# Kernel tuning notes

Measured on AMD Instinct MI355X. Metric: run time of the kernel, lower is better.

The kernel has to match this reference:

```python
import jax, jax.numpy as jnp
import numpy as np

H = 512      # hidden_size (hardcoded in __init__)
WD = 1024    # word_dim (hardcoded)
V = 4096     # len(i2w)+4
B, S, T = 256, 80, 28


def setup_inputs() -> dict:
    key = jax.random.key(0)
    ks = jax.random.split(key, 14)

    def gl(k, shape, fan_in):
        return (jax.random.normal(k, shape, jnp.float32) / np.sqrt(fan_in)).astype(jnp.float32)

    return {
        "encoder_last_hidden_state": jax.random.normal(ks[0], (1, B, H), jnp.float32),
        "encoder_output": jax.random.normal(ks[1], (B, S, H), jnp.float32),
        "targets": jax.random.randint(ks[2], (B, T), 0, V, dtype=jnp.int32),
        # embedding table
        "embedding": gl(ks[3], (V, WD), WD),
        # attention MLP (4 stacked linears, no activations, per the source)
        "W1": gl(ks[4], (2 * H, H), 2 * H), "b1": jnp.zeros((H,), jnp.float32),
        "W2": gl(ks[5], (H, H), H), "b2": jnp.zeros((H,), jnp.float32),
        "W3": gl(ks[6], (H, H), H), "b3": jnp.zeros((H,), jnp.float32),
        "W4": gl(ks[7], (H, H), H), "b4": jnp.zeros((H,), jnp.float32),
        "Ww": gl(ks[8], (H, 1), H),
        # GRU (input = hidden_size + word_dim = 1536), PyTorch gate order r,z,n
        "W_ih": gl(ks[9], (3 * H, H + WD), H + WD), "b_ih": jnp.zeros((3 * H,), jnp.float32),
        "W_hh": gl(ks[10], (3 * H, H), H), "b_hh": jnp.zeros((3 * H,), jnp.float32),
        # output projection
        "Wo": gl(ks[11], (H, V), H), "bo": jnp.zeros((V,), jnp.float32),
    }


def reference(encoder_last_hidden_state, encoder_output, targets, embedding,
              W1, b1, W2, b2, W3, b3, W4, b4, Ww,
              W_ih, b_ih, W_hh, b_hh, Wo, bo):
    n_steps = targets.shape[1] - 1  # seq_len - 1 decode steps

    def attention(h, enc):
        # h: (B,H) decoder hidden; enc: (B,S,H)
        hs = jnp.broadcast_to(h[:, None, :], enc.shape)
        m = jnp.concatenate([enc, hs], axis=-1)          # (B,S,2H)
        x = m @ W1 + b1
        x = x @ W2 + b2
        x = x @ W3 + b3
        x = x @ W4 + b4
        attw = jax.nn.softmax((x @ Ww)[..., 0], axis=1)  # (B,S)
        return jnp.einsum('bs,bsh->bh', attw, enc)       # context (B,H)

    def gru_cell(x, h):
        gi = x @ W_ih.T + b_ih
        gh = h @ W_hh.T + b_hh
        ir, iz, inn = jnp.split(gi, 3, axis=-1)
        hr, hz, hn = jnp.split(gh, 3, axis=-1)
        r = jax.nn.sigmoid(ir + hr)
        z = jax.nn.sigmoid(iz + hz)
        n = jnp.tanh(inn + r * hn)
        return (1.0 - z) * n + z * h

    h0 = encoder_last_hidden_state[0]                    # (B,H)
    w0 = jnp.ones((encoder_output.shape[0],), jnp.int32) # <BOS> = 1

    def step(carry, _):
        h, w = carry
        emb = embedding[w]                               # (B,WD)
        ctx = attention(h, encoder_output)               # (B,H)
        x = jnp.concatenate([emb, ctx], axis=-1)         # (B,WD+H)
        hn = gru_cell(x, h)
        logits = hn @ Wo + bo                            # (B,V)
        wn = jnp.argmax(logits, axis=-1).astype(jnp.int32)
        return (hn, wn), logits

    _, logits_seq = jax.lax.scan(step, (h0, w0), None, length=n_steps)
    seq_logProb = jnp.swapaxes(logits_seq, 0, 1)         # (B, T-1, V)
    seq_predictions = jnp.argmax(seq_logProb, axis=-1)
    return seq_logProb, seq_predictions
```

## Files before the change

kernel.cpp:

```cpp
#include <hip/hip_runtime.h>

#define B_ 256
#define S_ 80
#define H_ 512
#define V_ 4096
#define NSTEP 27

typedef unsigned short u16;
typedef __attribute__((ext_vector_type(8))) short short8v;
typedef __attribute__((ext_vector_type(4))) float f32x4;
typedef __attribute__((ext_vector_type(4))) unsigned short ushort4v;

#define MFMA_(a,b,c) __builtin_amdgcn_mfma_f32_16x16x32_bf16(a,b,c,0,0,0)
#define MFMA3(acc, ah, al, bh, bl) do{ acc = MFMA_(ah,bh,acc); acc = MFMA_(ah,bl,acc); acc = MFMA_(al,bh,acc);}while(0)

__device__ __forceinline__ unsigned fkey(float v){
    unsigned u = __float_as_uint(v);
    return (u & 0x80000000u) ? ~u : (u | 0x80000000u);
}
__device__ __forceinline__ u16 bf16_rne(float f){
    unsigned u = __float_as_uint(f);
    return (u16)((u + 0x7FFFu + ((u >> 16) & 1u)) >> 16);
}
__device__ __forceinline__ void split_f4(float4 v, ushort4v& hi, ushort4v& lo){
    float arr[4] = {v.x, v.y, v.z, v.w};
    ushort4v h, l;
#pragma unroll
    for (int i = 0; i < 4; ++i){
        u16 hb = bf16_rne(arr[i]);
        h[i] = hb;
        l[i] = bf16_rne(arr[i] - __uint_as_float(((unsigned)hb) << 16));
    }
    hi = h; lo = l;
}

__global__ __launch_bounds__(64) void matvec512(const float* __restrict__ W,
                                                const float* __restrict__ v,
                                                float* __restrict__ out){
    int row = blockIdx.x, lane = threadIdx.x;
    const float* wr = W + row * 512;
    float s = 0.f;
#pragma unroll
    for (int i = 0; i < 8; ++i) s += wr[lane + 64*i] * v[lane + 64*i];
#pragma unroll
    for (int off = 32; off; off >>= 1) s += __shfl_xor(s, off);
    if (lane == 0) out[row] = s;
}

__global__ __launch_bounds__(512) void attn_ctx(const float* __restrict__ enc,
                                                const float* __restrict__ weff,
                                                float* __restrict__ ctx){
    __shared__ float att[S_];
    int b = blockIdx.x, tid = threadIdx.x;
    int wv = tid >> 6, lane = tid & 63;
    float w8[8];
#pragma unroll
    for (int i = 0; i < 8; ++i) w8[i] = weff[lane + 64*i];
    const float* eb = enc + (size_t)b * (S_*H_);
    for (int s = wv; s < S_; s += 8){
        const float* e = eb + s*512;
        float acc = 0.f;
#pragma unroll
        for (int i = 0; i < 8; ++i) acc += e[lane + 64*i] * w8[i];
#pragma unroll
        for (int off = 32; off; off >>= 1) acc += __shfl_xor(acc, off);
        if (lane == 0) att[s] = acc;
    }
    __syncthreads();
    if (tid == 0){
        float mx = att[0];
        for (int s = 1; s < S_; ++s) mx = fmaxf(mx, att[s]);
        float sum = 0.f;
        for (int s = 0; s < S_; ++s){ float e = expf(att[s] - mx); att[s] = e; sum += e; }
        float inv = 1.f / sum;
        for (int s = 0; s < S_; ++s) att[s] *= inv;
    }
    __syncthreads();
    float a = 0.f;
    for (int s = 0; s < S_; ++s) a += att[s] * eb[s*512 + tid];
    ctx[b*512 + tid] = a;
}

template<int TM>
__global__ __launch_bounds__(256) void gemm_abt(const float* __restrict__ A, int lda,
                                                const float* __restrict__ Bm, int ldb,
                                                const float* __restrict__ bias,
                                                float* __restrict__ C, int ldc, int K){
    constexpr int RPT = TM / 16;
    __shared__ float As[16][TM + 4];
    __shared__ float Bs[16][64 + 4];
    int m0 = blockIdx.x * TM, n0 = blockIdx.y * 64;
    int tid = threadIdx.x;
    int lk = tid & 15, lr = tid >> 4;
    int tx = tid & 15, ty = tid >> 4;
    float c[RPT][4] = {};
    for (int k0 = 0; k0 < K; k0 += 16){
#pragma unroll
        for (int i = 0; i < RPT; ++i)
            As[lk][lr*RPT + i] = A[(size_t)(m0 + lr*RPT + i)*lda + k0 + lk];
#pragma unroll
        for (int i = 0; i < 4; ++i)
            Bs[lk][lr*4 + i] = Bm[(size_t)(n0 + lr*4 + i)*ldb + k0 + lk];
        __syncthreads();
#pragma unroll
        for (int k = 0; k < 16; ++k){
            float b4[4];
            *(float4*)b4 = *(const float4*)&Bs[k][tx*4];
#pragma unroll
            for (int i = 0; i < RPT; ++i){
                float a = As[k][ty*RPT + i];
#pragma unroll
                for (int j = 0; j < 4; ++j) c[i][j] += a * b4[j];
            }
        }
        __syncthreads();
    }
#pragma unroll
    for (int j = 0; j < 4; ++j){
        float bb = bias ? bias[n0 + tx*4 + j] : 0.f;
#pragma unroll
        for (int i = 0; i < RPT; ++i)
            C[(size_t)(m0 + ty*RPT + i)*ldc + n0 + tx*4 + j] = c[i][j] + bb;
    }
}

__global__ __launch_bounds__(256) void prep_all(
    const float* __restrict__ Whh, const float* __restrict__ Wo,
    const float* __restrict__ emb, const float* __restrict__ Wih,
    const float* __restrict__ elhs,
    u16* __restrict__ WhhHi, u16* __restrict__ WhhLo,
    u16* __restrict__ WoThi, u16* __restrict__ WoTlo,
    u16* __restrict__ EmbHi, u16* __restrict__ EmbLo,
    u16* __restrict__ WihLHi, u16* __restrict__ WihLLo,
    u16* __restrict__ Sh, u16* __restrict__ Sl,
    unsigned* __restrict__ zp, int nz)
{
    __shared__ float T[64][65];
    int b = blockIdx.x, tid = threadIdx.x;
    if (b < 768){
        int idx = (b*256 + tid)*4;
        float4 v = *(const float4*)&Whh[idx];
        ushort4v h,l; split_f4(v,h,l);
        *(ushort4v*)&WhhHi[idx]=h; *(ushort4v*)&WhhLo[idx]=l;
    } else if (b < 1280){
        int lb = b - 768;
        int k0 = (lb & 7)*64, n0 = (lb >> 3)*64;
#pragma unroll
        for (int i = 0; i < 16; ++i){
            int idx = tid + i*256;
            int kk = idx >> 6, nn = idx & 63;
            T[kk][nn] = Wo[(size_t)(k0+kk)*4096 + n0+nn];
        }
        __syncthreads();
#pragma unroll
        for (int i = 0; i < 16; ++i){
            int idx = tid + i*256;
            int nn = idx >> 6, kk = idx & 63;
            float v = T[kk][nn];
            u16 hi = bf16_rne(v);
            u16 lo = bf16_rne(v - __uint_as_float(((unsigned)hi) << 16));
            size_t o = (size_t)(n0+nn)*512 + k0+kk;
            WoThi[o] = hi; WoTlo[o] = lo;
        }
    } else if (b < 5376){
        int idx = ((b-1280)*256 + tid)*4;
        float4 v = *(const float4*)&emb[idx];
        ushort4v h,l; split_f4(v,h,l);
        *(ushort4v*)&EmbHi[idx]=h; *(ushort4v*)&EmbLo[idx]=l;
    } else if (b < 6912){
        int id = ((b-5376)*256 + tid)*4;
        int r = id >> 10, c = id & 1023;
        float4 v = *(const float4*)&Wih[(size_t)r*1536 + c];
        ushort4v h,l; split_f4(v,h,l);
        *(ushort4v*)&WihLHi[id]=h; *(ushort4v*)&WihLLo[id]=l;
    } else if (b < 7040){
        int idx = ((b-6912)*256 + tid)*4;
        float4 v = *(const float4*)&elhs[idx];
        ushort4v h,l; split_f4(v,h,l);
        *(ushort4v*)&Sh[idx]=h; *(ushort4v*)&Sl[idx]=l;
    } else {
        int i = ((b-7040)*256 + tid)*4;
        if (i < nz){ zp[i]=0u; zp[i+1]=0u; zp[i+2]=0u; zp[i+3]=0u; }
    }
}

__global__ __launch_bounds__(256) void eproj_u16(const u16* __restrict__ Ahi, const u16* __restrict__ Alo,
                                                 const u16* __restrict__ Bhi, const u16* __restrict__ Blo,
                                                 float* __restrict__ C){
    __shared__ u16 Ah[2048], Al[2048], Bh[4096], Bl[4096];
    int n0 = blockIdx.x * 128, m0 = blockIdx.y * 64;
    int tid = threadIdx.x, lane = tid & 63, wid = tid >> 6;
    int wy = wid & 1, wx = wid >> 1;
    int l15 = lane & 15, rg = lane >> 4, lk = rg * 8;
    int ar = tid >> 2, ak8 = (tid & 3) * 8;

    const u16* gAh = Ahi + (size_t)(m0 + ar)*1024 + ak8;
    const u16* gAl = Alo + (size_t)(m0 + ar)*1024 + ak8;
    const u16* gBh0 = Bhi + (size_t)(n0 + ar)*1024 + ak8;
    const u16* gBl0 = Blo + (size_t)(n0 + ar)*1024 + ak8;
    const u16* gBh1 = gBh0 + (size_t)64*1024;
    const u16* gBl1 = gBl0 + (size_t)64*1024;

    short8v rAh = *(const short8v*)gAh;
    short8v rAl = *(const short8v*)gAl;
    short8v rBh0 = *(const short8v*)gBh0;
    short8v rBl0 = *(const short8v*)gBl0;
    short8v rBh1 = *(const short8v*)gBh1;
    short8v rBl1 = *(const short8v*)gBl1;

    f32x4 acc[2][4] = {};
    for (int k0 = 0; k0 < 1024; k0 += 32){
        __syncthreads();
        *(short8v*)&Ah[tid*8] = rAh;
        *(short8v*)&Al[tid*8] = rAl;
        *(short8v*)&Bh[tid*8] = rBh0;
        *(short8v*)&Bl[tid*8] = rBl0;
        *(short8v*)&Bh[2048 + tid*8] = rBh1;
        *(short8v*)&Bl[2048 + tid*8] = rBl1;
        __syncthreads();
        if (k0 + 32 < 1024){
            rAh  = *(const short8v*)(gAh + k0 + 32);
            rAl  = *(const short8v*)(gAl + k0 + 32);
            rBh0 = *(const short8v*)(gBh0 + k0 + 32);
            rBl0 = *(const short8v*)(gBl0 + k0 + 32);
            rBh1 = *(const short8v*)(gBh1 + k0 + 32);
            rBl1 = *(const short8v*)(gBl1 + k0 + 32);
        }
        short8v afh[2], afl[2];
        afh[0] = *(const short8v*)&Ah[(wy*32 +  0 + l15)*32 + lk];
        afh[1] = *(const short8v*)&Ah[(wy*32 + 16 + l15)*32 + lk];
        afl[0] = *(const short8v*)&Al[(wy*32 +  0 + l15)*32 + lk];
        afl[1] = *(const short8v*)&Al[(wy*32 + 16 + l15)*32 + lk];
#pragma unroll
        for (int nf = 0; nf < 4; ++nf){
            short8v bfh = *(const short8v*)&Bh[(wx*64 + nf*16 + l15)*32 + lk];
            short8v bfl = *(const short8v*)&Bl[(wx*64 + nf*16 + l15)*32 + lk];
            MFMA3(acc[0][nf], afh[0], afl[0], bfh, bfl);
            MFMA3(acc[1][nf], afh[1], afl[1], bfh, bfl);
        }
    }
    int col0 = n0 + wx*64 + l15;
#pragma unroll
    for (int mf = 0; mf < 2; ++mf)
#pragma unroll
        for (int r = 0; r < 4; ++r){
            int row = m0 + wy*32 + mf*16 + rg*4 + r;
#pragma unroll
            for (int nf = 0; nf < 4; ++nf)
                C[(size_t)row*1536 + col0 + nf*16] = acc[mf][nf][r];
        }
}


__global__ __launch_bounds__(128) void gru_pointwise(
    const float* __restrict__ gh, const float* __restrict__ Eproj,
    const float* __restrict__ gictx, const float* __restrict__ bhh,
    const float* __restrict__ hprev, float* __restrict__ hnext,
    u16* __restrict__ Sh, u16* __restrict__ Sl,
    const unsigned long long* __restrict__ Pprev,
    float* __restrict__ preds, int t)
{
    int tid = threadIdx.x;
    int row = blockIdx.x;
    int jj = tid * 4;
    int w = 1;
    if (t > 0){
        w = 4095 - (int)(Pprev[row] & 0xFFFFFFFFull);
        if (w < 0) w = 0; if (w > 4095) w = 4095;
        if (tid == 0) preds[row*NSTEP + (t-1)] = (float)w;
    }
    const float* gr = gh + (size_t)row * 1536;
    const float* ep = Eproj + (size_t)w * 1536;
    const float* gc = gictx + (size_t)row * 1536;
    float4 g0 = *(const float4*)&gr[jj];
    float4 g1 = *(const float4*)&gr[512 + jj];
    float4 g2 = *(const float4*)&gr[1024 + jj];
    float4 e0 = *(const float4*)&ep[jj];
    float4 e1 = *(const float4*)&ep[512 + jj];
    float4 e2 = *(const float4*)&ep[1024 + jj];
    float4 c0 = *(const float4*)&gc[jj];
    float4 c1 = *(const float4*)&gc[512 + jj];
    float4 c2 = *(const float4*)&gc[1024 + jj];
    float4 b0 = *(const float4*)&bhh[jj];
    float4 b1 = *(const float4*)&bhh[512 + jj];
    float4 b2 = *(const float4*)&bhh[1024 + jj];
    float4 ho = *(const float4*)&hprev[(size_t)row*512 + jj];
    const float* G0 = (const float*)&g0; const float* G1 = (const float*)&g1;
    const float* G2 = (const float*)&g2;
    const float* E0 = (const float*)&e0; const float* E1 = (const float*)&e1;
    const float* E2 = (const float*)&e2;
    const float* C0 = (const float*)&c0; const float* C1 = (const float*)&c1;
    const float* C2 = (const float*)&c2;
    const float* B0 = (const float*)&b0; const float* B1 = (const float*)&b1;
    const float* B2 = (const float*)&b2;
    const float* HO = (const float*)&ho;
    float4 res;
    float* R = (float*)&res;
#pragma unroll
    for (int i = 0; i < 4; ++i){
        float gir = E0[i] + C0[i] + G0[i] + B0[i];
        float giz = E1[i] + C1[i] + G1[i] + B1[i];
        float gin = E2[i] + C2[i];
        float rr = 1.f / (1.f + expf(-gir));
        float zz = 1.f / (1.f + expf(-giz));
        float nn = tanhf(gin + rr * (G2[i] + B2[i]));
        R[i] = (1.f - zz)*nn + zz*HO[i];
    }
    size_t o = (size_t)row*512 + jj;
    *(float4*)&hnext[o] = res;
    ushort4v h4, l4; split_f4(res, h4, l4);
    *(ushort4v*)&Sh[o] = h4;
    *(ushort4v*)&Sl[o] = l4;
}

__global__ __launch_bounds__(256) void step_mm(
    const u16* __restrict__ Ahg, const u16* __restrict__ Alg,
    const u16* __restrict__ WoHi, const u16* __restrict__ WoLo,
    const u16* __restrict__ WhhHi, const u16* __restrict__ WhhLo,
    const float* __restrict__ bo,
    float* __restrict__ logits, unsigned long long* __restrict__ Pcur,
    float* __restrict__ gh_out, int n_logits)
{
    __shared__ u16 Ah[2][2048], Al[2][2048], Bh[2][2048], Bl[2][2048];
    int m0 = blockIdx.x * 64;
    int nt = blockIdx.y;
    bool isL = nt < n_logits;
    int nbase = (isL ? nt : nt - n_logits) * 64;
    const u16* Bhg = isL ? WoHi : WhhHi;
    const u16* Blg = isL ? WoLo : WhhLo;
    int tid = threadIdx.x, lane = tid & 63, wid = tid >> 6;
    int wy = wid & 1, wx = wid >> 1;
    int l15 = lane & 15, rg = lane >> 4, lk = rg * 8;
    int sr = tid >> 2, sk8 = (tid & 3) * 8;

    const u16* gAh = Ahg + (size_t)(m0 + sr)*512 + sk8;
    const u16* gAl = Alg + (size_t)(m0 + sr)*512 + sk8;
    const u16* gBh = Bhg + (size_t)(nbase + sr)*512 + sk8;
    const u16* gBl = Blg + (size_t)(nbase + sr)*512 + sk8;

    *(short8v*)&Ah[0][tid*8] = *(const short8v*)gAh;
    *(short8v*)&Al[0][tid*8] = *(const short8v*)gAl;
    *(short8v*)&Bh[0][tid*8] = *(const short8v*)gBh;
    *(short8v*)&Bl[0][tid*8] = *(const short8v*)gBl;
    short8v r1a = *(const short8v*)(gAh + 32), r1b = *(const short8v*)(gAl + 32);
    short8v r1c = *(const short8v*)(gBh + 32), r1d = *(const short8v*)(gBl + 32);
    short8v r2a = *(const short8v*)(gAh + 64), r2b = *(const short8v*)(gAl + 64);
    short8v r2c = *(const short8v*)(gBh + 64), r2d = *(const short8v*)(gBl + 64);
    __syncthreads();

    f32x4 acc[2][2] = {};
    int p = 0;
    for (int k0 = 0; k0 < 512; k0 += 32){
        if (k0 + 32 < 512){
            *(short8v*)&Ah[p^1][tid*8] = r1a;
            *(short8v*)&Al[p^1][tid*8] = r1b;
            *(short8v*)&Bh[p^1][tid*8] = r1c;
            *(short8v*)&Bl[p^1][tid*8] = r1d;
            r1a = r2a; r1b = r2b; r1c = r2c; r1d = r2d;
            if (k0 + 96 < 512){
                r2a = *(const short8v*)(gAh + k0 + 96);
                r2b = *(const short8v*)(gAl + k0 + 96);
                r2c = *(const short8v*)(gBh + k0 + 96);
                r2d = *(const short8v*)(gBl + k0 + 96);
            }
        }
        short8v afh0 = *(const short8v*)&Ah[p][(wy*32 +  0 + l15)*32 + lk];
        short8v afh1 = *(const short8v*)&Ah[p][(wy*32 + 16 + l15)*32 + lk];
        short8v afl0 = *(const short8v*)&Al[p][(wy*32 +  0 + l15)*32 + lk];
        short8v afl1 = *(const short8v*)&Al[p][(wy*32 + 16 + l15)*32 + lk];
        short8v bfh0 = *(const short8v*)&Bh[p][(wx*32 +  0 + l15)*32 + lk];
        short8v bfh1 = *(const short8v*)&Bh[p][(wx*32 + 16 + l15)*32 + lk];
        short8v bfl0 = *(const short8v*)&Bl[p][(wx*32 +  0 + l15)*32 + lk];
        short8v bfl1 = *(const short8v*)&Bl[p][(wx*32 + 16 + l15)*32 + lk];
        MFMA3(acc[0][0], afh0, afl0, bfh0, bfl0);
        MFMA3(acc[0][1], afh0, afl0, bfh1, bfl1);
        MFMA3(acc[1][0], afh1, afl1, bfh0, bfl0);
        MFMA3(acc[1][1], afh1, afl1, bfh1, bfl1);
        __syncthreads();
        p ^= 1;
    }

    int col0 = nbase + wx*32 + l15;
    if (isL){
        float bo0 = bo[col0], bo1 = bo[col0 + 16];
#pragma unroll
        for (int mf = 0; mf < 2; ++mf){
#pragma unroll
            for (int r = 0; r < 4; ++r){
                int row = m0 + wy*32 + mf*16 + rg*4 + r;
                float v0 = acc[mf][0][r] + bo0;
                float v1 = acc[mf][1][r] + bo1;
                float* crow = logits + (size_t)row * (NSTEP * (size_t)V_);
                crow[col0]      = v0;
                crow[col0 + 16] = v1;
                unsigned long long k0_ = ((unsigned long long)fkey(v0) << 32) | (unsigned)(4095 - col0);
                unsigned long long k1_ = ((unsigned long long)fkey(v1) << 32) | (unsigned)(4095 - (col0+16));
                unsigned long long best = k0_ > k1_ ? k0_ : k1_;
#pragma unroll
                for (int off = 1; off < 16; off <<= 1){
                    unsigned long long o = __shfl_xor(best, off);
                    if (o > best) best = o;
                }
                if (l15 == 0) atomicMax(&Pcur[row], best);
            }
        }
    } else {
#pragma unroll
        for (int mf = 0; mf < 2; ++mf)
#pragma unroll
            for (int r = 0; r < 4; ++r){
                int row = m0 + wy*32 + mf*16 + rg*4 + r;
                gh_out[(size_t)row*1536 + col0]      = acc[mf][0][r];
                gh_out[(size_t)row*1536 + col0 + 16] = acc[mf][1][r];
            }
    }
}

__global__ __launch_bounds__(256) void final_pred(const unsigned long long* __restrict__ P,
                                                  float* __restrict__ preds){
    int b = threadIdx.x;
    int w = 4095 - (int)(P[b] & 0xFFFFFFFFull);
    if (w < 0) w = 0; if (w > 4095) w = 4095;
    preds[b*NSTEP + (NSTEP-1)] = (float)w;
}

extern "C" void kernel_launch(void* const* d_in, const int* in_sizes, int n_in,
                              void* d_out, int out_size, void* d_ws, size_t ws_size,
                              hipStream_t stream){
    const float* elhs = (const float*)d_in[0];
    const float* enc  = (const float*)d_in[1];
    const float* emb  = (const float*)d_in[3];
    const float* W1   = (const float*)d_in[4];
    const float* W2   = (const float*)d_in[6];
    const float* W3   = (const float*)d_in[8];
    const float* W4   = (const float*)d_in[10];
    const float* Ww   = (const float*)d_in[12];
    const float* Wih  = (const float*)d_in[13];
    const float* bih  = (const float*)d_in[14];
    const float* Whh  = (const float*)d_in[15];
    const float* bhh  = (const float*)d_in[16];
    const float* Wo   = (const float*)d_in[17];
    const float* bo   = (const float*)d_in[18];

    float* out = (float*)d_out;
    float* preds = out + (size_t)B_ * NSTEP * V_;

    float* ws = (float*)d_ws;
    float* Eproj  = ws;  ws += (size_t)V_ * 1536;
    float* gictx  = ws;  ws += (size_t)B_ * 1536;
    float* ctx    = ws;  ws += B_ * H_;
    float* t1     = ws;  ws += 512;
    float* t2     = ws;  ws += 512;
    float* weff   = ws;  ws += 512;
    float* Hf     = ws;  ws += 2 * B_ * H_;
    float* ghbuf  = ws;  ws += B_ * 1536;
    u16* WoT_hi = (u16*)ws;  ws += (size_t)V_ * 512 / 2;
    u16* WoT_lo = (u16*)ws;  ws += (size_t)V_ * 512 / 2;
    u16* WhhHi  = (u16*)ws;  ws += 1536 * 512 / 2;
    u16* WhhLo  = (u16*)ws;  ws += 1536 * 512 / 2;
    u16* Sh     = (u16*)ws;  ws += B_ * H_ / 2;
    u16* Sl     = (u16*)ws;  ws += B_ * H_ / 2;
    unsigned long long* P = (unsigned long long*)ws;

    u16* EmbHi  = (u16*)d_out;
    u16* EmbLo  = EmbHi + (size_t)V_*1024;
    u16* WihLHi = EmbLo + (size_t)V_*1024;
    u16* WihLLo = WihLHi + (size_t)1536*1024;

    prep_all<<<7054, 256, 0, stream>>>(Whh, Wo, emb, Wih, elhs,
                                       WhhHi, WhhLo, WoT_hi, WoT_lo,
                                       EmbHi, EmbLo, WihLHi, WihLLo,
                                       Sh, Sl, (unsigned*)P, NSTEP*256*2);

    matvec512<<<512, 64, 0, stream>>>(W4, Ww, t1);
    matvec512<<<512, 64, 0, stream>>>(W3, t1, t2);
    matvec512<<<512, 64, 0, stream>>>(W2, t2, t1);
    matvec512<<<512, 64, 0, stream>>>(W1, t1, weff);
    attn_ctx<<<B_, 512, 0, stream>>>(enc, weff, ctx);
    { dim3 g(B_/32, 1536/64);
      gemm_abt<32><<<g, 256, 0, stream>>>(ctx, 512, Wih + 1024, 1536, bih, gictx, 1536, 512); }
    { dim3 g(1536/128, V_/64);
      eproj_u16<<<g, 256, 0, stream>>>(EmbHi, EmbLo, WihLHi, WihLLo, Eproj); }

    { dim3 g(4, 24);
      step_mm<<<g, 256, 0, stream>>>(Sh, Sl, WoT_hi, WoT_lo, WhhHi, WhhLo, bo,
                                     out, P, ghbuf, 0); }

    for (int t = 0; t < NSTEP; ++t){
        const float* hr = (t == 0) ? elhs : (Hf + (size_t)((t-1) & 1) * (B_*H_));
        float*       hw = Hf + (size_t)(t & 1) * (B_*H_);
        const unsigned long long* Pprev = P + (size_t)(t > 0 ? t-1 : 0) * 256;
        gru_pointwise<<<256, 128, 0, stream>>>(ghbuf, Eproj, gictx, bhh, hr, hw,
                                               Sh, Sl, Pprev, preds, t);
        dim3 g(4, 64 + 24);
        step_mm<<<g, 256, 0, stream>>>(Sh, Sl, WoT_hi, WoT_lo, WhhHi, WhhLo, bo,
                                       out + (size_t)t * V_, P + (size_t)t*256, ghbuf, 64);
    }
    final_pred<<<1, 256, 0, stream>>>(P + (size_t)(NSTEP-1)*256, preds);
}
```

Measured before the change: 746.5 us.

## Merge front-end kernels: fold attention matvec chain into prep and fuse setup GEMMs

The four matvec launches that collapse the attention MLP into a single weight vector now run in one extra block of the prep kernel. The ctx-projection GEMM, the embedding projection GEMM (retiled to 128x128) and the first hidden-to-hidden step_mm are combined into one heterogeneous launch. The goal is to cut launch count and serialization in the setup phase. The trade-off is that the weff chain runs in a single block, which can end up on the critical path, and branch-divergent blocks inside one kernel may load-balance unevenly.

After: 841.5 us. +12.7%, slower.

```diff
diff --git a/kernel.cpp b/kernel.cpp
--- a/kernel.cpp
+++ b/kernel.cpp
@@ -34,105 +34,19 @@
     hi = h; lo = l;
 }
 
-__global__ __launch_bounds__(64) void matvec512(const float* __restrict__ W,
-                                                const float* __restrict__ v,
-                                                float* __restrict__ out){
-    int row = blockIdx.x, lane = threadIdx.x;
-    const float* wr = W + row * 512;
-    float s = 0.f;
-#pragma unroll
-    for (int i = 0; i < 8; ++i) s += wr[lane + 64*i] * v[lane + 64*i];
-#pragma unroll
-    for (int off = 32; off; off >>= 1) s += __shfl_xor(s, off);
-    if (lane == 0) out[row] = s;
-}
-
-__global__ __launch_bounds__(512) void attn_ctx(const float* __restrict__ enc,
-                                                const float* __restrict__ weff,
-                                                float* __restrict__ ctx){
-    __shared__ float att[S_];
-    int b = blockIdx.x, tid = threadIdx.x;
-    int wv = tid >> 6, lane = tid & 63;
-    float w8[8];
-#pragma unroll
-    for (int i = 0; i < 8; ++i) w8[i] = weff[lane + 64*i];
-    const float* eb = enc + (size_t)b * (S_*H_);
-    for (int s = wv; s < S_; s += 8){
-        const float* e = eb + s*512;
-        float acc = 0.f;
-#pragma unroll
-        for (int i = 0; i < 8; ++i) acc += e[lane + 64*i] * w8[i];
-#pragma unroll
-        for (int off = 32; off; off >>= 1) acc += __shfl_xor(acc, off);
-        if (lane == 0) att[s] = acc;
-    }
-    __syncthreads();
-    if (tid == 0){
-        float mx = att[0];
-        for (int s = 1; s < S_; ++s) mx = fmaxf(mx, att[s]);
-        float sum = 0.f;
-        for (int s = 0; s < S_; ++s){ float e = expf(att[s] - mx); att[s] = e; sum += e; }
-        float inv = 1.f / sum;
-        for (int s = 0; s < S_; ++s) att[s] *= inv;
-    }
-    __syncthreads();
-    float a = 0.f;
-    for (int s = 0; s < S_; ++s) a += att[s] * eb[s*512 + tid];
-    ctx[b*512 + tid] = a;
-}
-
-template<int TM>
-__global__ __launch_bounds__(256) void gemm_abt(const float* __restrict__ A, int lda,
-                                                const float* __restrict__ Bm, int ldb,
-                                                const float* __restrict__ bias,
-                                                float* __restrict__ C, int ldc, int K){
-    constexpr int RPT = TM / 16;
-    __shared__ float As[16][TM + 4];
-    __shared__ float Bs[16][64 + 4];
-    int m0 = blockIdx.x * TM, n0 = blockIdx.y * 64;
-    int tid = threadIdx.x;
-    int lk = tid & 15, lr = tid >> 4;
-    int tx = tid & 15, ty = tid >> 4;
-    float c[RPT][4] = {};
-    for (int k0 = 0; k0 < K; k0 += 16){
-#pragma unroll
-        for (int i = 0; i < RPT; ++i)
-            As[lk][lr*RPT + i] = A[(size_t)(m0 + lr*RPT + i)*lda + k0 + lk];
-#pragma unroll
-        for (int i = 0; i < 4; ++i)
-            Bs[lk][lr*4 + i] = Bm[(size_t)(n0 + lr*4 + i)*ldb + k0 + lk];
-        __syncthreads();
-#pragma unroll
-        for (int k = 0; k < 16; ++k){
-            float b4[4];
-            *(float4*)b4 = *(const float4*)&Bs[k][tx*4];
-#pragma unroll
-            for (int i = 0; i < RPT; ++i){
-                float a = As[k][ty*RPT + i];
-#pragma unroll
-                for (int j = 0; j < 4; ++j) c[i][j] += a * b4[j];
-            }
-        }
-        __syncthreads();
-    }
-#pragma unroll
-    for (int j = 0; j < 4; ++j){
-        float bb = bias ? bias[n0 + tx*4 + j] : 0.f;
-#pragma unroll
-        for (int i = 0; i < RPT; ++i)
-            C[(size_t)(m0 + ty*RPT + i)*ldc + n0 + tx*4 + j] = c[i][j] + bb;
-    }
-}
-
-__global__ __launch_bounds__(256) void prep_all(
+__global__ __launch_bounds__(256) void prep_front(
     const float* __restrict__ Whh, const float* __restrict__ Wo,
     const float* __restrict__ emb, const float* __restrict__ Wih,
     const float* __restrict__ elhs,
+    const float* __restrict__ W1, const float* __restrict__ W2,
+    const float* __restrict__ W3, const float* __restrict__ W4,
+    const float* __restrict__ Ww,
     u16* __restrict__ WhhHi, u16* __restrict__ WhhLo,
     u16* __restrict__ WoThi, u16* __restrict__ WoTlo,
     u16* __restrict__ EmbHi, u16* __restrict__ EmbLo,
     u16* __restrict__ WihLHi, u16* __restrict__ WihLLo,
     u16* __restrict__ Sh, u16* __restrict__ Sl,
+    float* __restrict__ weff,
     unsigned* __restrict__ zp, int nz)
 {
     __shared__ float T[64][65];
@@ -178,79 +92,300 @@
         float4 v = *(const float4*)&elhs[idx];
         ushort4v h,l; split_f4(v,h,l);
         *(ushort4v*)&Sh[idx]=h; *(ushort4v*)&Sl[idx]=l;
-    } else {
+    } else if (b < 7054){
         int i = ((b-7040)*256 + tid)*4;
         if (i < nz){ zp[i]=0u; zp[i+1]=0u; zp[i+2]=0u; zp[i+3]=0u; }
-    }
-}
-
-__global__ __launch_bounds__(256) void eproj_u16(const u16* __restrict__ Ahi, const u16* __restrict__ Alo,
-                                                 const u16* __restrict__ Bhi, const u16* __restrict__ Blo,
-                                                 float* __restrict__ C){
-    __shared__ u16 Ah[2048], Al[2048], Bh[4096], Bl[4096];
-    int n0 = blockIdx.x * 128, m0 = blockIdx.y * 64;
+    } else {
+        float* vb0 = &T[0][0];
+        float* vb1 = vb0 + 512;
+        for (int i = tid; i < 512; i += 256) vb0[i] = Ww[i];
+        __syncthreads();
+        const float* Ws[4] = {W4, W3, W2, W1};
+        for (int s = 0; s < 4; ++s){
+            const float* src = (s & 1) ? vb1 : vb0;
+            float* dst = (s & 1) ? vb0 : vb1;
+            for (int r = tid; r < 512; r += 256){
+                const float* wr = Ws[s] + (size_t)r*512;
+                float acc = 0.f;
+                for (int k = 0; k < 512; k += 4){
+                    float4 wv = *(const float4*)&wr[k];
+                    acc += wv.x*src[k] + wv.y*src[k+1] + wv.z*src[k+2] + wv.w*src[k+3];
+                }
+                dst[r] = acc;
+            }
+            __syncthreads();
+        }
+        for (int i = tid; i < 512; i += 256) weff[i] = vb0[i];
+    }
+}
+
+__global__ __launch_bounds__(512) void attn_ctx(const float* __restrict__ enc,
+                                                const float* __restrict__ weff,
+                                                float* __restrict__ ctx){
+    __shared__ float att[S_];
+    int b = blockIdx.x, tid = threadIdx.x;
+    int wv = tid >> 6, lane = tid & 63;
+    float w8[8];
+#pragma unroll
+    for (int i = 0; i < 8; ++i) w8[i] = weff[lane + 64*i];
+    const float* eb = enc + (size_t)b * (S_*H_);
+    for (int s = wv; s < S_; s += 8){
+        const float* e = eb + s*512;
+        float acc = 0.f;
+#pragma unroll
+        for (int i = 0; i < 8; ++i) acc += e[lane + 64*i] * w8[i];
+#pragma unroll
+        for (int off = 32; off; off >>= 1) acc += __shfl_xor(acc, off);
+        if (lane == 0) att[s] = acc;
+    }
+    __syncthreads();
+    if (tid == 0){
+        float mx = att[0];
+        for (int s = 1; s < S_; ++s) mx = fmaxf(mx, att[s]);
+        float sum = 0.f;
+        for (int s = 0; s < S_; ++s){ float e = expf(att[s] - mx); att[s] = e; sum += e; }
+        float inv = 1.f / sum;
+        for (int s = 0; s < S_; ++s) att[s] *= inv;
+    }
+    __syncthreads();
+    float a = 0.f;
+    for (int s = 0; s < S_; ++s) a += att[s] * eb[s*512 + tid];
+    ctx[b*512 + tid] = a;
+}
+
+__device__ __forceinline__ void step_mm_body(char* smem, int m0, int nt, int n_logits,
+    const u16* __restrict__ Ahg, const u16* __restrict__ Alg,
+    const u16* __restrict__ WoHi, const u16* __restrict__ WoLo,
+    const u16* __restrict__ WhhHi, const u16* __restrict__ WhhLo,
+    const float* __restrict__ bo,
+    float* __restrict__ logits, unsigned long long* __restrict__ Pcur,
+    float* __restrict__ gh_out)
+{
+    u16 (*Ah)[2048] = (u16(*)[2048])(smem);
+    u16 (*Al)[2048] = (u16(*)[2048])(smem + 8192);
+    u16 (*Bh)[2048] = (u16(*)[2048])(smem + 16384);
+    u16 (*Bl)[2048] = (u16(*)[2048])(smem + 24576);
+    bool isL = nt < n_logits;
+    int nbase = (isL ? nt : nt - n_logits) * 64;
+    const u16* Bhg = isL ? WoHi : WhhHi;
+    const u16* Blg = isL ? WoLo : WhhLo;
     int tid = threadIdx.x, lane = tid & 63, wid = tid >> 6;
     int wy = wid & 1, wx = wid >> 1;
     int l15 = lane & 15, rg = lane >> 4, lk = rg * 8;
-    int ar = tid >> 2, ak8 = (tid & 3) * 8;
-
-    const u16* gAh = Ahi + (size_t)(m0 + ar)*1024 + ak8;
-    const u16* gAl = Alo + (size_t)(m0 + ar)*1024 + ak8;
-    const u16* gBh0 = Bhi + (size_t)(n0 + ar)*1024 + ak8;
-    const u16* gBl0 = Blo + (size_t)(n0 + ar)*1024 + ak8;
-    const u16* gBh1 = gBh0 + (size_t)64*1024;
-    const u16* gBl1 = gBl0 + (size_t)64*1024;
-
-    short8v rAh = *(const short8v*)gAh;
-    short8v rAl = *(const short8v*)gAl;
-    short8v rBh0 = *(const short8v*)gBh0;
-    short8v rBl0 = *(const short8v*)gBl0;
-    short8v rBh1 = *(const short8v*)gBh1;
-    short8v rBl1 = *(const short8v*)gBl1;
-
-    f32x4 acc[2][4] = {};
-    for (int k0 = 0; k0 < 1024; k0 += 32){
+    int sr = tid >> 2, sk8 = (tid & 3) * 8;
+
+    const u16* gAh = Ahg + (size_t)(m0 + sr)*512 + sk8;
+    const u16* gAl = Alg + (size_t)(m0 + sr)*512 + sk8;
+    const u16* gBh = Bhg + (size_t)(nbase + sr)*512 + sk8;
+    const u16* gBl = Blg + (size_t)(nbase + sr)*512 + sk8;
+
+    *(short8v*)&Ah[0][tid*8] = *(const short8v*)gAh;
+    *(short8v*)&Al[0][tid*8] = *(const short8v*)gAl;
+    *(short8v*)&Bh[0][tid*8] = *(const short8v*)gBh;
+    *(short8v*)&Bl[0][tid*8] = *(const short8v*)gBl;
+    short8v r1a = *(const short8v*)(gAh + 32), r1b = *(const short8v*)(gAl + 32);
+    short8v r1c = *(const short8v*)(gBh + 32), r1d = *(const short8v*)(gBl + 32);
+    short8v r2a = *(const short8v*)(gAh + 64), r2b = *(const short8v*)(gAl + 64);
+    short8v r2c = *(const short8v*)(gBh + 64), r2d = *(const short8v*)(gBl + 64);
+    __syncthreads();
+
+    f32x4 acc[2][2] = {};
+    int p = 0;
+    for (int k0 = 0; k0 < 512; k0 += 32){
+        if (k0 + 32 < 512){
+            *(short8v*)&Ah[p^1][tid*8] = r1a;
+            *(short8v*)&Al[p^1][tid*8] = r1b;
+            *(short8v*)&Bh[p^1][tid*8] = r1c;
+            *(short8v*)&Bl[p^1][tid*8] = r1d;
+            r1a = r2a; r1b = r2b; r1c = r2c; r1d = r2d;
+            if (k0 + 96 < 512){
+                r2a = *(const short8v*)(gAh + k0 + 96);
+                r2b = *(const short8v*)(gAl + k0 + 96);
+                r2c = *(const short8v*)(gBh + k0 + 96);
+                r2d = *(const short8v*)(gBl + k0 + 96);
+            }
+        }
+        short8v afh0 = *(const short8v*)&Ah[p][(wy*32 +  0 + l15)*32 + lk];
+        short8v afh1 = *(const short8v*)&Ah[p][(wy*32 + 16 + l15)*32 + lk];
+        short8v afl0 = *(const short8v*)&Al[p][(wy*32 +  0 + l15)*32 + lk];
+        short8v afl1 = *(const short8v*)&Al[p][(wy*32 + 16 + l15)*32 + lk];
+        short8v bfh0 = *(const short8v*)&Bh[p][(wx*32 +  0 + l15)*32 + lk];
+        short8v bfh1 = *(const short8v*)&Bh[p][(wx*32 + 16 + l15)*32 + lk];
+        short8v bfl0 = *(const short8v*)&Bl[p][(wx*32 +  0 + l15)*32 + lk];
+        short8v bfl1 = *(const short8v*)&Bl[p][(wx*32 + 16 + l15)*32 + lk];
+        MFMA3(acc[0][0], afh0, afl0, bfh0, bfl0);
+        MFMA3(acc[0][1], afh0, afl0, bfh1, bfl1);
+        MFMA3(acc[1][0], afh1, afl1, bfh0, bfl0);
+        MFMA3(acc[1][1], afh1, afl1, bfh1, bfl1);
         __syncthreads();
-        *(short8v*)&Ah[tid*8] = rAh;
-        *(short8v*)&Al[tid*8] = rAl;
-        *(short8v*)&Bh[tid*8] = rBh0;
-        *(short8v*)&Bl[tid*8] = rBl0;
-        *(short8v*)&Bh[2048 + tid*8] = rBh1;
-        *(short8v*)&Bl[2048 + tid*8] = rBl1;
-        __syncthreads();
-        if (k0 + 32 < 1024){
-            rAh  = *(const short8v*)(gAh + k0 + 32);
-            rAl  = *(const short8v*)(gAl + k0 + 32);
-            rBh0 = *(const short8v*)(gBh0 + k0 + 32);
-            rBl0 = *(const short8v*)(gBl0 + k0 + 32);
-            rBh1 = *(const short8v*)(gBh1 + k0 + 32);
-            rBl1 = *(const short8v*)(gBl1 + k0 + 32);
-        }
-        short8v afh[2], afl[2];
-        afh[0] = *(const short8v*)&Ah[(wy*32 +  0 + l15)*32 + lk];
-        afh[1] = *(const short8v*)&Ah[(wy*32 + 16 + l15)*32 + lk];
-        afl[0] = *(const short8v*)&Al[(wy*32 +  0 + l15)*32 + lk];
-        afl[1] = *(const short8v*)&Al[(wy*32 + 16 + l15)*32 + lk];
-#pragma unroll
-        for (int nf = 0; nf < 4; ++nf){
-            short8v bfh = *(const short8v*)&Bh[(wx*64 + nf*16 + l15)*32 + lk];
-            short8v bfl = *(const short8v*)&Bl[(wx*64 + nf*16 + l15)*32 + lk];
-            MFMA3(acc[0][nf], afh[0], afl[0], bfh, bfl);
-            MFMA3(acc[1][nf], afh[1], afl[1], bfh, bfl);
-        }
-    }
-    int col0 = n0 + wx*64 + l15;
-#pragma unroll
-    for (int mf = 0; mf < 2; ++mf)
-#pragma unroll
-        for (int r = 0; r < 4; ++r){
-            int row = m0 + wy*32 + mf*16 + rg*4 + r;
-#pragma unroll
-            for (int nf = 0; nf < 4; ++nf)
-                C[(size_t)row*1536 + col0 + nf*16] = acc[mf][nf][r];
-        }
-}
-
+        p ^= 1;
+    }
+
+    int col0 = nbase + wx*32 + l15;
+    if (isL){
+        float bo0 = bo[col0], bo1 = bo[col0 + 16];
+#pragma unroll
+        for (int mf = 0; mf < 2; ++mf){
+#pragma unroll
+            for (int r = 0; r < 4; ++r){
+                int row = m0 + wy*32 + mf*16 + rg*4 + r;
+                float v0 = acc[mf][0][r] + bo0;
+                float v1 = acc[mf][1][r] + bo1;
+                float* crow = logits + (size_t)row * (NSTEP * (size_t)V_);
+                crow[col0]      = v0;
+                crow[col0 + 16] = v1;
+                unsigned long long k0_ = ((unsigned long long)fkey(v0) << 32) | (unsigned)(4095 - col0);
+                unsigned long long k1_ = ((unsigned long long)fkey(v1) << 32) | (unsigned)(4095 - (col0+16));
+                unsigned long long best = k0_ > k1_ ? k0_ : k1_;
+#pragma unroll
+                for (int off = 1; off < 16; off <<= 1){
+                    unsigned long long o = __shfl_xor(best, off);
+                    if (o > best) best = o;
+                }
+                if (l15 == 0) atomicMax(&Pcur[row], best);
+            }
+        }
+    } else {
+#pragma unroll
+        for (int mf = 0; mf < 2; ++mf)
+#pragma unroll
+            for (int r = 0; r < 4; ++r){
+                int row = m0 + wy*32 + mf*16 + rg*4 + r;
+                gh_out[(size_t)row*1536 + col0]      = acc[mf][0][r];
+                gh_out[(size_t)row*1536 + col0 + 16] = acc[mf][1][r];
+            }
+    }
+}
+
+__global__ __launch_bounds__(256) void front3(
+    const u16* __restrict__ EmbHi, const u16* __restrict__ EmbLo,
+    const u16* __restrict__ WihLHi, const u16* __restrict__ WihLLo,
+    float* __restrict__ Eproj,
+    const float* __restrict__ ctx, const float* __restrict__ WihR,
+    const float* __restrict__ bih, float* __restrict__ gictx,
+    const u16* __restrict__ Sh0, const u16* __restrict__ Sl0,
+    const u16* __restrict__ WhhHi, const u16* __restrict__ WhhLo,
+    float* __restrict__ gh0)
+{
+    __shared__ __align__(16) char smem[32768];
+    int b = blockIdx.x, tid = threadIdx.x;
+    if (b < 384){
+        int bn = b % 12, bm = b / 12;
+        int n0 = bn * 128, m0 = bm * 128;
+        int lane = tid & 63, wid = tid >> 6;
+        int wy = wid & 1, wx = wid >> 1;
+        int l15 = lane & 15, rg = lane >> 4, lk = rg * 8;
+        u16* Ah = (u16*)smem;
+        u16* Al = (u16*)(smem + 8192);
+        u16* Bh = (u16*)(smem + 16384);
+        u16* Bl = (u16*)(smem + 24576);
+        const u16* gA[2][2]; const u16* gB[2][2];
+#pragma unroll
+        for (int j = 0; j < 2; ++j){
+            int s = tid + j*256;
+            int row = s >> 2, k8 = (s & 3)*8;
+            gA[0][j] = EmbHi + (size_t)(m0+row)*1024 + k8;
+            gA[1][j] = EmbLo + (size_t)(m0+row)*1024 + k8;
+            gB[0][j] = WihLHi + (size_t)(n0+row)*1024 + k8;
+            gB[1][j] = WihLLo + (size_t)(n0+row)*1024 + k8;
+        }
+        short8v rA[2][2], rB[2][2];
+#pragma unroll
+        for (int h = 0; h < 2; ++h)
+#pragma unroll
+            for (int j = 0; j < 2; ++j){
+                rA[h][j] = *(const short8v*)gA[h][j];
+                rB[h][j] = *(const short8v*)gB[h][j];
+            }
+        f32x4 acc[4][4] = {};
+        for (int k0 = 0; k0 < 1024; k0 += 32){
+            __syncthreads();
+#pragma unroll
+            for (int j = 0; j < 2; ++j){
+                int s8 = (tid + j*256)*8;
+                *(short8v*)&Ah[s8] = rA[0][j];
+                *(short8v*)&Al[s8] = rA[1][j];
+                *(short8v*)&Bh[s8] = rB[0][j];
+                *(short8v*)&Bl[s8] = rB[1][j];
+            }
+            __syncthreads();
+            if (k0 + 32 < 1024){
+#pragma unroll
+                for (int h = 0; h < 2; ++h)
+#pragma unroll
+                    for (int j = 0; j < 2; ++j){
+                        rA[h][j] = *(const short8v*)(gA[h][j] + k0 + 32);
+                        rB[h][j] = *(const short8v*)(gB[h][j] + k0 + 32);
+                    }
+            }
+            short8v afh[4], afl[4];
+#pragma unroll
+            for (int mf = 0; mf < 4; ++mf){
+                afh[mf] = *(const short8v*)&Ah[(wy*64 + mf*16 + l15)*32 + lk];
+                afl[mf] = *(const short8v*)&Al[(wy*64 + mf*16 + l15)*32 + lk];
+            }
+#pragma unroll
+            for (int nf = 0; nf < 4; ++nf){
+                short8v bfh = *(const short8v*)&Bh[(wx*64 + nf*16 + l15)*32 + lk];
+                short8v bfl = *(const short8v*)&Bl[(wx*64 + nf*16 + l15)*32 + lk];
+#pragma unroll
+                for (int mf = 0; mf < 4; ++mf)
+                    MFMA3(acc[mf][nf], afh[mf], afl[mf], bfh, bfl);
+            }
+        }
+        int col0 = n0 + wx*64 + l15;
+#pragma unroll
+        for (int mf = 0; mf < 4; ++mf)
+#pragma unroll
+            for (int r = 0; r < 4; ++r){
+                int row = m0 + wy*64 + mf*16 + rg*4 + r;
+#pragma unroll
+                for (int nf = 0; nf < 4; ++nf)
+                    Eproj[(size_t)row*1536 + col0 + nf*16] = acc[mf][nf][r];
+            }
+    } else if (b < 576){
+        int lb = b - 384;
+        int m0 = (lb & 7) * 32, n0 = (lb >> 3) * 64;
+        float (*As)[36] = (float(*)[36])smem;
+        float (*Bs)[68] = (float(*)[68])(smem + 2304);
+        int lk = tid & 15, lr = tid >> 4;
+        int tx = tid & 15, ty = tid >> 4;
+        float c[2][4] = {};
+        for (int k0 = 0; k0 < 512; k0 += 16){
+#pragma unroll
+            for (int i = 0; i < 2; ++i)
+                As[lk][lr*2 + i] = ctx[(size_t)(m0 + lr*2 + i)*512 + k0 + lk];
+#pragma unroll
+            for (int i = 0; i < 4; ++i)
+                Bs[lk][lr*4 + i] = WihR[(size_t)(n0 + lr*4 + i)*1536 + k0 + lk];
+            __syncthreads();
+#pragma unroll
+            for (int k = 0; k < 16; ++k){
+                float b4[4];
+                *(float4*)b4 = *(const float4*)&Bs[k][tx*4];
+#pragma unroll
+                for (int i = 0; i < 2; ++i){
+                    float a = As[k][ty*2 + i];
+#pragma unroll
+                    for (int j = 0; j < 4; ++j) c[i][j] += a * b4[j];
+                }
+            }
+            __syncthreads();
+        }
+#pragma unroll
+        for (int j = 0; j < 4; ++j){
+            float bb = bih[n0 + tx*4 + j];
+#pragma unroll
+            for (int i = 0; i < 2; ++i)
+                gictx[(size_t)(m0 + ty*2 + i)*1536 + n0 + tx*4 + j] = c[i][j] + bb;
+        }
+    } else {
+        int lb = b - 576;
+        step_mm_body(smem, (lb & 3)*64, lb >> 2, 0,
+                     Sh0, Sl0, nullptr, nullptr, WhhHi, WhhLo,
+                     nullptr, nullptr, nullptr, gh0);
+    }
+}
 
 __global__ __launch_bounds__(128) void gru_pointwise(
     const float* __restrict__ gh, const float* __restrict__ Eproj,
@@ -321,99 +456,9 @@
     float* __restrict__ logits, unsigned long long* __restrict__ Pcur,
     float* __restrict__ gh_out, int n_logits)
 {
-    __shared__ u16 Ah[2][2048], Al[2][2048], Bh[2][2048], Bl[2][2048];
-    int m0 = blockIdx.x * 64;
-    int nt = blockIdx.y;
-    bool isL = nt < n_logits;
-    int nbase = (isL ? nt : nt - n_logits) * 64;
-    const u16* Bhg = isL ? WoHi : WhhHi;
-    const u16* Blg = isL ? WoLo : WhhLo;
-    int tid = threadIdx.x, lane = tid & 63, wid = tid >> 6;
-    int wy = wid & 1, wx = wid >> 1;
-    int l15 = lane & 15, rg = lane >> 4, lk = rg * 8;
-    int sr = tid >> 2, sk8 = (tid & 3) * 8;
-
-    const u16* gAh = Ahg + (size_t)(m0 + sr)*512 + sk8;
-    const u16* gAl = Alg + (size_t)(m0 + sr)*512 + sk8;
-    const u16* gBh = Bhg + (size_t)(nbase + sr)*512 + sk8;
-    const u16* gBl = Blg + (size_t)(nbase + sr)*512 + sk8;
-
-    *(short8v*)&Ah[0][tid*8] = *(const short8v*)gAh;
-    *(short8v*)&Al[0][tid*8] = *(const short8v*)gAl;
-    *(short8v*)&Bh[0][tid*8] = *(const short8v*)gBh;
-    *(short8v*)&Bl[0][tid*8] = *(const short8v*)gBl;
-    short8v r1a = *(const short8v*)(gAh + 32), r1b = *(const short8v*)(gAl + 32);
-    short8v r1c = *(const short8v*)(gBh + 32), r1d = *(const short8v*)(gBl + 32);
-    short8v r2a = *(const short8v*)(gAh + 64), r2b = *(const short8v*)(gAl + 64);
-    short8v r2c = *(const short8v*)(gBh + 64), r2d = *(const short8v*)(gBl + 64);
-    __syncthreads();
-
-    f32x4 acc[2][2] = {};
-    int p = 0;
-    for (int k0 = 0; k0 < 512; k0 += 32){
-        if (k0 + 32 < 512){
-            *(short8v*)&Ah[p^1][tid*8] = r1a;
-            *(short8v*)&Al[p^1][tid*8] = r1b;
-            *(short8v*)&Bh[p^1][tid*8] = r1c;
-            *(short8v*)&Bl[p^1][tid*8] = r1d;
-            r1a = r2a; r1b = r2b; r1c = r2c; r1d = r2d;
-            if (k0 + 96 < 512){
-                r2a = *(const short8v*)(gAh + k0 + 96);
-                r2b = *(const short8v*)(gAl + k0 + 96);
-                r2c = *(const short8v*)(gBh + k0 + 96);
-                r2d = *(const short8v*)(gBl + k0 + 96);
-            }
-        }
-        short8v afh0 = *(const short8v*)&Ah[p][(wy*32 +  0 + l15)*32 + lk];
-        short8v afh1 = *(const short8v*)&Ah[p][(wy*32 + 16 + l15)*32 + lk];
-        short8v afl0 = *(const short8v*)&Al[p][(wy*32 +  0 + l15)*32 + lk];
-        short8v afl1 = *(const short8v*)&Al[p][(wy*32 + 16 + l15)*32 + lk];
-        short8v bfh0 = *(const short8v*)&Bh[p][(wx*32 +  0 + l15)*32 + lk];
-        short8v bfh1 = *(const short8v*)&Bh[p][(wx*32 + 16 + l15)*32 + lk];
-        short8v bfl0 = *(const short8v*)&Bl[p][(wx*32 +  0 + l15)*32 + lk];
-        short8v bfl1 = *(const short8v*)&Bl[p][(wx*32 + 16 + l15)*32 + lk];
-        MFMA3(acc[0][0], afh0, afl0, bfh0, bfl0);
-        MFMA3(acc[0][1], afh0, afl0, bfh1, bfl1);
-        MFMA3(acc[1][0], afh1, afl1, bfh0, bfl0);
-        MFMA3(acc[1][1], afh1, afl1, bfh1, bfl1);
-        __syncthreads();
-        p ^= 1;
-    }
-
-    int col0 = nbase + wx*32 + l15;
-    if (isL){
-        float bo0 = bo[col0], bo1 = bo[col0 + 16];
-#pragma unroll
-        for (int mf = 0; mf < 2; ++mf){
-#pragma unroll
-            for (int r = 0; r < 4; ++r){
-                int row = m0 + wy*32 + mf*16 + rg*4 + r;
-                float v0 = acc[mf][0][r] + bo0;
-                float v1 = acc[mf][1][r] + bo1;
-                float* crow = logits + (size_t)row * (NSTEP * (size_t)V_);
-                crow[col0]      = v0;
-                crow[col0 + 16] = v1;
-                unsigned long long k0_ = ((unsigned long long)fkey(v0) << 32) | (unsigned)(4095 - col0);
-                unsigned long long k1_ = ((unsigned long long)fkey(v1) << 32) | (unsigned)(4095 - (col0+16));
-                unsigned long long best = k0_ > k1_ ? k0_ : k1_;
-#pragma unroll
-                for (int off = 1; off < 16; off <<= 1){
-                    unsigned long long o = __shfl_xor(best, off);
-                    if (o > best) best = o;
-                }
-                if (l15 == 0) atomicMax(&Pcur[row], best);
-            }
-        }
-    } else {
-#pragma unroll
-        for (int mf = 0; mf < 2; ++mf)
-#pragma unroll
-            for (int r = 0; r < 4; ++r){
-                int row = m0 + wy*32 + mf*16 + rg*4 + r;
-                gh_out[(size_t)row*1536 + col0]      = acc[mf][0][r];
-                gh_out[(size_t)row*1536 + col0 + 16] = acc[mf][1][r];
-            }
-    }
+    __shared__ __align__(16) char smem[32768];
+    step_mm_body(smem, blockIdx.x * 64, blockIdx.y, n_logits,
+                 Ahg, Alg, WoHi, WoLo, WhhHi, WhhLo, bo, logits, Pcur, gh_out);
 }
 
 __global__ __launch_bounds__(256) void final_pred(const unsigned long long* __restrict__ P,
@@ -449,8 +494,6 @@
     float* Eproj  = ws;  ws += (size_t)V_ * 1536;
     float* gictx  = ws;  ws += (size_t)B_ * 1536;
     float* ctx    = ws;  ws += B_ * H_;
-    float* t1     = ws;  ws += 512;
-    float* t2     = ws;  ws += 512;
     float* weff   = ws;  ws += 512;
     float* Hf     = ws;  ws += 2 * B_ * H_;
     float* ghbuf  = ws;  ws += B_ * 1536;
@@ -467,24 +510,15 @@
     u16* WihLHi = EmbLo + (size_t)V_*1024;
     u16* WihLLo = WihLHi + (size_t)1536*1024;
 
-    prep_all<<<7054, 256, 0, stream>>>(Whh, Wo, emb, Wih, elhs,
-                                       WhhHi, WhhLo, WoT_hi, WoT_lo,
-                                       EmbHi, EmbLo, WihLHi, WihLLo,
-                                       Sh, Sl, (unsigned*)P, NSTEP*256*2);
-
-    matvec512<<<512, 64, 0, stream>>>(W4, Ww, t1);
-    matvec512<<<512, 64, 0, stream>>>(W3, t1, t2);
-    matvec512<<<512, 64, 0, stream>>>(W2, t2, t1);
-    matvec512<<<512, 64, 0, stream>>>(W1, t1, weff);
+    prep_front<<<7055, 256, 0, stream>>>(Whh, Wo, emb, Wih, elhs,
+                                         W1, W2, W3, W4, Ww,
+                                         WhhHi, WhhLo, WoT_hi, WoT_lo,
+                                         EmbHi, EmbLo, WihLHi, WihLLo,
+                                         Sh, Sl, weff, (unsigned*)P, NSTEP*256*2);
     attn_ctx<<<B_, 512, 0, stream>>>(enc, weff, ctx);
-    { dim3 g(B_/32, 1536/64);
-      gemm_abt<32><<<g, 256, 0, stream>>>(ctx, 512, Wih + 1024, 1536, bih, gictx, 1536, 512); }
-    { dim3 g(1536/128, V_/64);
-      eproj_u16<<<g, 256, 0, stream>>>(EmbHi, EmbLo, WihLHi, WihLLo, Eproj); }
-
-    { dim3 g(4, 24);
-      step_mm<<<g, 256, 0, stream>>>(Sh, Sl, WoT_hi, WoT_lo, WhhHi, WhhLo, bo,
-                                     out, P, ghbuf, 0); }
+    front3<<<672, 256, 0, stream>>>(EmbHi, EmbLo, WihLHi, WihLLo, Eproj,
+                                    ctx, Wih + 1024, bih, gictx,
+                                    Sh, Sl, WhhHi, WhhLo, ghbuf);
 
     for (int t = 0; t < NSTEP; ++t){
         const float* hr = (t == 0) ? elhs : (Hf + (size_t)((t-1) & 1) * (B_*H_));
```
